# Performance work log

Measured on AMD Instinct MI355X. Metric: run time of the kernel, lower is better.

Reference implementation:

```python
import math
import jax, jax.numpy as jnp
import numpy as np

B, S, HID = 1, 2048, 2880
H, HKV, D = 64, 8, 64
G = H // HKV  # num_key_value_groups = 8


def setup_inputs() -> dict:
    key = jax.random.key(0)
    ks = jax.random.split(key, 10)
    sd = 1.0 / math.sqrt(HID)
    hidden_states = jax.random.normal(ks[0], (B, S, HID), dtype=jnp.float32)
    # causal additive mask [B, 1, S, S]
    causal = jnp.tril(jnp.ones((S, S), dtype=bool))
    attention_mask = jnp.where(causal, 0.0, -1e9).astype(jnp.float32)[None, None]
    Wq = jax.random.normal(ks[1], (H * D, HID), dtype=jnp.float32) * sd
    bq = jax.random.normal(ks[2], (H * D,), dtype=jnp.float32) * 0.01
    Wk = jax.random.normal(ks[3], (HKV * D, HID), dtype=jnp.float32) * sd
    bk = jax.random.normal(ks[4], (HKV * D,), dtype=jnp.float32) * 0.01
    Wv = jax.random.normal(ks[5], (HKV * D, HID), dtype=jnp.float32) * sd
    bv = jax.random.normal(ks[6], (HKV * D,), dtype=jnp.float32) * 0.01
    Wo = jax.random.normal(ks[7], (HID, H * D), dtype=jnp.float32) * (1.0 / math.sqrt(H * D))
    bo = jax.random.normal(ks[8], (HID,), dtype=jnp.float32) * 0.01
    return {"hidden_states": hidden_states, "attention_mask": attention_mask,
            "Wq": Wq, "bq": bq, "Wk": Wk, "bk": bk, "Wv": Wv, "bv": bv,
            "Wo": Wo, "bo": bo}


def reference(hidden_states, attention_mask, Wq, bq, Wk, bk, Wv, bv, Wo, bo):
    b, s, _ = hidden_states.shape
    # projections
    q = hidden_states @ Wq.T + bq  # [b, s, H*D]
    k = hidden_states @ Wk.T + bk  # [b, s, HKV*D]
    v = hidden_states @ Wv.T + bv
    # torch q head index h maps to kv head h // G, so split H -> (HKV, G)
    q = q.reshape(b, s, HKV, G, D).transpose(0, 2, 3, 1, 4)   # [b, kv, g, s, d]
    k = k.reshape(b, s, HKV, D).transpose(0, 2, 1, 3)         # [b, kv, s, d]
    v = v.reshape(b, s, HKV, D).transpose(0, 2, 1, 3)
    # grouped-query attention without materializing repeated KV (same math as repeat_interleave)
    scores = jnp.einsum('bkgsd,bktd->bkgst', q, k) / math.sqrt(D)
    scores = scores + attention_mask[:, :, None]              # broadcast [b,1,1,s,t]
    attn = jax.nn.softmax(scores.astype(jnp.float32), axis=-1).astype(q.dtype)
    out = jnp.einsum('bkgst,bktd->bkgsd', attn, v)            # [b, kv, g, s, d]
    out = out.transpose(0, 3, 1, 2, 4).reshape(b, s, H * D)
    return out @ Wo.T + bo
```

## Files before the change

kernel.cpp:

```cpp
#include <hip/hip_runtime.h>
#include <hip/hip_bf16.h>
#include <cmath>

typedef __hip_bfloat16 bf16;
typedef __bf16 bf16x8 __attribute__((ext_vector_type(8)));
typedef float floatx4 __attribute__((ext_vector_type(4)));

__device__ inline floatx4 mfma16(bf16x8 a, bf16x8 b, floatx4 c) {
  return __builtin_amdgcn_mfma_f32_16x16x32_bf16(a, b, c, 0, 0, 0);
}

__device__ inline void async_ld16(const void* g, void* l) {
  __builtin_amdgcn_global_load_lds((const __attribute__((address_space(1))) void*)g,
                                   (__attribute__((address_space(3))) void*)l,
                                   16, 0, 0);
}

__device__ inline uint4 pack8(float4 a, float4 b) {
  union { uint4 u; bf16 h[8]; } t;
  t.h[0] = __float2bfloat16(a.x); t.h[1] = __float2bfloat16(a.y);
  t.h[2] = __float2bfloat16(a.z); t.h[3] = __float2bfloat16(a.w);
  t.h[4] = __float2bfloat16(b.x); t.h[5] = __float2bfloat16(b.y);
  t.h[6] = __float2bfloat16(b.z); t.h[7] = __float2bfloat16(b.w);
  return t.u;
}

__global__ __launch_bounds__(256)
void cvt_f32_bf16(const float* __restrict__ s, bf16* __restrict__ d, int n8) {
  const int i = blockIdx.x * 256 + threadIdx.x;
  if (i >= n8) return;
  const float4 a = ((const float4*)s)[2 * i];
  const float4 b = ((const float4*)s)[2 * i + 1];
  ((uint4*)d)[i] = pack8(a, b);
}

__global__ void concat_bias3(const float* __restrict__ q, const float* __restrict__ k,
                             const float* __restrict__ v, float* __restrict__ o) {
  const int i = blockIdx.x * 256 + threadIdx.x;
  if (i < 4096) o[i] = q[i];
  else if (i < 4608) o[i] = k[i - 4096];
  else o[i] = v[i - 4608];
}

#define QSCALE 0.1803368801111601f

template <int A_BF, int B_BF, int OUT_MODE>
__global__ __launch_bounds__(256)
void gemm_bt_bias(const void* __restrict__ Ap, const void* __restrict__ Bp,
                  const float* __restrict__ bias, void* __restrict__ Cp,
                  void* __restrict__ Cqp, void* __restrict__ Ctp,
                  int M, int N, int K, float qmul) {
  __shared__ __align__(16) bf16 sA[128 * 32];
  __shared__ __align__(16) bf16 sB[128 * 32];
  const int tid  = threadIdx.x;
  const int wave = tid >> 6;
  const int lane = tid & 63;
  const int quad = lane >> 4;
  const int l15  = lane & 15;
  const int bm = blockIdx.y * 128;
  const int bn = blockIdx.x * 128;
  const int wm = (wave & 1) * 64;
  const int wn = (wave >> 1) * 64;

  floatx4 acc[4][4] = {};

  const int g0 = tid, g1 = tid + 256;
  const int arow0 = bm + (g0 >> 2), acol0 = (g0 & 3) * 8;
  const int arow1 = bm + (g1 >> 2), acol1 = (g1 & 3) * 8;
  int brow0 = bn + (g0 >> 2); if (brow0 >= N) brow0 = N - 1;
  int brow1 = bn + (g1 >> 2); if (brow1 >= N) brow1 = N - 1;

  for (int k0 = 0; k0 < K; k0 += 32) {
    __syncthreads();
    if (A_BF) {
      const bf16* A = (const bf16*)Ap;
      async_ld16(A + (size_t)arow0 * K + k0 + acol0, sA + wave * 512);
      async_ld16(A + (size_t)arow1 * K + k0 + acol1, sA + 2048 + wave * 512);
    } else {
      const float* A = (const float*)Ap;
      const float* p0 = A + (size_t)arow0 * K + k0 + acol0;
      const float* p1 = A + (size_t)arow1 * K + k0 + acol1;
      *(uint4*)(sA + tid * 8)        = pack8(*(const float4*)p0, *(const float4*)(p0 + 4));
      *(uint4*)(sA + 2048 + tid * 8) = pack8(*(const float4*)p1, *(const float4*)(p1 + 4));
    }
    if (B_BF) {
      const bf16* B = (const bf16*)Bp;
      async_ld16(B + (size_t)brow0 * K + k0 + acol0, sB + wave * 512);
      async_ld16(B + (size_t)brow1 * K + k0 + acol1, sB + 2048 + wave * 512);
    } else {
      const float* B = (const float*)Bp;
      const float* p0 = B + (size_t)brow0 * K + k0 + acol0;
      const float* p1 = B + (size_t)brow1 * K + k0 + acol1;
      *(uint4*)(sB + tid * 8)        = pack8(*(const float4*)p0, *(const float4*)(p0 + 4));
      *(uint4*)(sB + 2048 + tid * 8) = pack8(*(const float4*)p1, *(const float4*)(p1 + 4));
    }
    __syncthreads();

    bf16x8 aF[4], bF[4];
#pragma unroll
    for (int mi = 0; mi < 4; ++mi)
      aF[mi] = *(const bf16x8*)(sA + (wm + mi * 16 + l15) * 32 + quad * 8);
#pragma unroll
    for (int ni = 0; ni < 4; ++ni)
      bF[ni] = *(const bf16x8*)(sB + (wn + ni * 16 + l15) * 32 + quad * 8);
#pragma unroll
    for (int mi = 0; mi < 4; ++mi)
#pragma unroll
      for (int ni = 0; ni < 4; ++ni)
        acc[mi][ni] = mfma16(aF[mi], bF[ni], acc[mi][ni]);
  }

#pragma unroll
  for (int ni = 0; ni < 4; ++ni) {
    const int col = bn + wn + ni * 16 + l15;
    if (col >= N) continue;
    const float bv = bias[col];
#pragma unroll
    for (int mi = 0; mi < 4; ++mi) {
      const int row = bm + wm + mi * 16 + quad * 4;
#pragma unroll
      for (int r = 0; r < 4; ++r) {
        const float val = acc[mi][ni][r] + bv;
        if (OUT_MODE == 0) {
          ((bf16*)Cp)[(size_t)(row + r) * N + col] = __float2bfloat16(val * qmul);
        } else if (OUT_MODE == 1) {
          ((float*)Cp)[(size_t)(row + r) * N + col] = val;
        } else if (OUT_MODE == 2) {
          ((bf16*)Ctp)[(size_t)col * M + row + r] = __float2bfloat16(val);
        } else {
          if (col < 4096)      ((bf16*)Cp)[(size_t)(row + r) * 4096 + col] = __float2bfloat16(val * qmul);
          else if (col < 4608) ((bf16*)Cqp)[(size_t)(row + r) * 512 + (col - 4096)] = __float2bfloat16(val);
          else                 ((bf16*)Ctp)[(size_t)(col - 4608) * M + row + r] = __float2bfloat16(val);
        }
      }
    }
  }
}

__global__ __launch_bounds__(256)
void attn_fused(const bf16* __restrict__ Q, const bf16* __restrict__ Kc,
                const bf16* __restrict__ Vt, bf16* __restrict__ AO) {
  constexpr int HD = 4096, KD = 512, SEQ = 2048;
  constexpr float NEG = -1e30f;
  __shared__ __align__(16) bf16 sP[64 * 64];
  __shared__ __align__(16) bf16 sK[2][64 * 64];
  __shared__ __align__(16) bf16 sV[2][64 * 64];

  const int qb = (int)gridDim.x - 1 - blockIdx.x;
  const int h  = blockIdx.y;
  const int kvh = h >> 3;
  const int tid = threadIdx.x, wave = tid >> 6, lane = tid & 63;
  const int quad = lane >> 4, l15 = lane & 15;
  const int sq0 = qb * 64;

  const int lrow = lane >> 3;
  const int lgr  = (lane & 7) ^ lrow;

  bf16x8 qf[2];
#pragma unroll
  for (int ks = 0; ks < 2; ++ks)
    qf[ks] = *(const bf16x8*)(Q + (size_t)(sq0 + wave * 16 + l15) * HD + h * 64 + ks * 32 + quad * 8);

  bf16x8 onesf;
#pragma unroll
  for (int i = 0; i < 8; ++i) onesf[i] = (__bf16)1.0f;

#pragma unroll
  for (int i = 0; i < 2; ++i) {
    const int c = wave * 2 + i;
    async_ld16(Kc + (size_t)(c * 8 + lrow) * KD + kvh * 64 + lgr * 8, &sK[0][c * 512]);
    async_ld16(Vt + (size_t)(kvh * 64 + c * 8 + lrow) * SEQ + lgr * 8, &sV[0][c * 512]);
  }

  floatx4 o_acc[4] = {};
  floatx4 o_sum = {};
  float m_run = NEG;

  for (int kt = 0; kt <= qb; ++kt) {
    const int st0 = kt * 64;
    __syncthreads();

    if (kt < qb) {
      const int st1 = st0 + 64;
      const int nb = (kt + 1) & 1;
#pragma unroll
      for (int i = 0; i < 2; ++i) {
        const int c = wave * 2 + i;
        async_ld16(Kc + (size_t)(st1 + c * 8 + lrow) * KD + kvh * 64 + lgr * 8, &sK[nb][c * 512]);
        async_ld16(Vt + (size_t)(kvh * 64 + c * 8 + lrow) * SEQ + st1 + lgr * 8, &sV[nb][c * 512]);
      }
    }
    const bf16* kb = sK[kt & 1];
    const bf16* vb = sV[kt & 1];

    floatx4 s_acc[4] = {};
#pragma unroll
    for (int ks = 0; ks < 2; ++ks) {
#pragma unroll
      for (int ni = 0; ni < 4; ++ni) {
        const bf16x8 kF = *(const bf16x8*)(kb + (ni * 16 + l15) * 64 + (((ks * 4 + quad) ^ (l15 & 7)) * 8));
        s_acc[ni] = mfma16(kF, qf[ks], s_acc[ni]);
      }
    }

    if (kt == qb) {
      const int qloc = wave * 16 + l15;
#pragma unroll
      for (int ni = 0; ni < 4; ++ni)
#pragma unroll
        for (int r = 0; r < 4; ++r)
          if (ni * 16 + quad * 4 + r > qloc) s_acc[ni][r] = NEG;
    }

    float t0 = fmaxf(fmaxf(s_acc[0][0], s_acc[0][1]), fmaxf(s_acc[0][2], s_acc[0][3]));
    float t1 = fmaxf(fmaxf(s_acc[1][0], s_acc[1][1]), fmaxf(s_acc[1][2], s_acc[1][3]));
    float t2 = fmaxf(fmaxf(s_acc[2][0], s_acc[2][1]), fmaxf(s_acc[2][2], s_acc[2][3]));
    float t3 = fmaxf(fmaxf(s_acc[3][0], s_acc[3][1]), fmaxf(s_acc[3][2], s_acc[3][3]));
    float tm = fmaxf(fmaxf(t0, t1), fmaxf(t2, t3));
    tm = fmaxf(tm, __shfl_xor(tm, 16));
    tm = fmaxf(tm, __shfl_xor(tm, 32));

    if (!__all(tm - m_run <= 8.0f)) {
      const float mn = fmaxf(m_run, tm);
      const float alpha = exp2f(m_run - mn);
      m_run = mn;
#pragma unroll
      for (int r = 0; r < 4; ++r) o_sum[r] *= alpha;
#pragma unroll
      for (int di = 0; di < 4; ++di)
#pragma unroll
        for (int r = 0; r < 4; ++r) o_acc[di][r] *= alpha;
    }

    const int prow = wave * 16 + l15;
#pragma unroll
    for (int ni = 0; ni < 4; ++ni) {
      union { uint2 u; bf16 hh[4]; } pk;
#pragma unroll
      for (int r = 0; r < 4; ++r)
        pk.hh[r] = __float2bfloat16(exp2f(s_acc[ni][r] - m_run));
      const int g = ni * 2 + (quad >> 1);
      *(uint2*)(sP + prow * 64 + ((g ^ (l15 & 7)) * 8) + (quad & 1) * 4) = pk.u;
    }

#pragma unroll
    for (int ks = 0; ks < 2; ++ks) {
      const bf16x8 pF = *(const bf16x8*)(sP + prow * 64 + (((ks * 4 + quad) ^ (l15 & 7)) * 8));
#pragma unroll
      for (int di = 0; di < 4; ++di) {
        const bf16x8 vF = *(const bf16x8*)(vb + (di * 16 + l15) * 64 + (((ks * 4 + quad) ^ (l15 & 7)) * 8));
        o_acc[di] = mfma16(vF, pF, o_acc[di]);
      }
      o_sum = mfma16(onesf, pF, o_sum);
    }
  }

  const float inv = 1.0f / o_sum[0];
  const int row = sq0 + wave * 16 + l15;
#pragma unroll
  for (int di = 0; di < 4; ++di) {
    union { uint2 u; bf16 hh[4]; } pk;
#pragma unroll
    for (int r = 0; r < 4; ++r)
      pk.hh[r] = __float2bfloat16(o_acc[di][r] * inv);
    *(uint2*)(AO + (size_t)row * HD + h * 64 + di * 16 + quad * 4) = pk.u;
  }
}

extern "C" void kernel_launch(void* const* d_in, const int* in_sizes, int n_in,
                              void* d_out, int out_size, void* d_ws, size_t ws_size,
                              hipStream_t stream) {
  const float* X  = (const float*)d_in[0];
  const float* Wq = (const float*)d_in[2];
  const float* bq = (const float*)d_in[3];
  const float* Wk = (const float*)d_in[4];
  const float* bk = (const float*)d_in[5];
  const float* Wv = (const float*)d_in[6];
  const float* bv = (const float*)d_in[7];
  const float* Wo = (const float*)d_in[8];
  const float* bo = (const float*)d_in[9];
  float* out = (float*)d_out;

  char* ws = (char*)d_ws;
  bf16* Qb = (bf16*)(ws);
  bf16* Kb = (bf16*)(ws + 16777216);
  bf16* Vt = (bf16*)(ws + 18874368);
  bf16* AO = (bf16*)(ws + 20971520);
  bf16*  Xb   = (bf16*)(ws + 37748736);
  bf16*  Wall = (bf16*)(ws + 49545216);
  bf16*  Wob  = (bf16*)(ws + 79036416);
  float* ball = (float*)(ws + 102629376);
  const size_t NEED = 102649856;

  dim3 blk(256);
  if (ws_size >= NEED) {
    cvt_f32_bf16<<<dim3(2048 * 2880 / 8 / 256), blk, 0, stream>>>(X, Xb, 2048 * 2880 / 8);
    cvt_f32_bf16<<<dim3(4096 * 2880 / 8 / 256), blk, 0, stream>>>(Wq, Wall, 4096 * 2880 / 8);
    cvt_f32_bf16<<<dim3(512 * 2880 / 8 / 256),  blk, 0, stream>>>(Wk, Wall + (size_t)4096 * 2880, 512 * 2880 / 8);
    cvt_f32_bf16<<<dim3(512 * 2880 / 8 / 256),  blk, 0, stream>>>(Wv, Wall + (size_t)4608 * 2880, 512 * 2880 / 8);
    cvt_f32_bf16<<<dim3(2880 * 4096 / 8 / 256), blk, 0, stream>>>(Wo, Wob, 2880 * 4096 / 8);
    concat_bias3<<<dim3(20), blk, 0, stream>>>(bq, bk, bv, ball);

    gemm_bt_bias<1, 1, 4><<<dim3(40, 16), blk, 0, stream>>>(Xb, Wall, ball, Qb, Kb, Vt, 2048, 5120, 2880, QSCALE);
    attn_fused<<<dim3(32, 64), blk, 0, stream>>>(Qb, Kb, Vt, AO);
    gemm_bt_bias<1, 1, 1><<<dim3(23, 16), blk, 0, stream>>>(AO, Wob, bo, out, nullptr, nullptr, 2048, 2880, 4096, 1.f);
  } else {
    gemm_bt_bias<0, 0, 0><<<dim3(32, 16), blk, 0, stream>>>(X, Wq, bq, Qb, nullptr, nullptr, 2048, 4096, 2880, QSCALE);
    gemm_bt_bias<0, 0, 0><<<dim3(4, 16),  blk, 0, stream>>>(X, Wk, bk, Kb, nullptr, nullptr, 2048, 512, 2880, 1.f);
    gemm_bt_bias<0, 0, 2><<<dim3(4, 16),  blk, 0, stream>>>(X, Wv, bv, nullptr, nullptr, Vt, 2048, 512, 2880, 1.f);
    attn_fused<<<dim3(32, 64), blk, 0, stream>>>(Qb, Kb, Vt, AO);
    gemm_bt_bias<1, 0, 1><<<dim3(23, 16), blk, 0, stream>>>(AO, Wo, bo, out, nullptr, nullptr, 2048, 2880, 4096, 1.f);
  }
}
```

Baseline: 513.0 us.

## Add double-buffered bf16 GEMM with XCD-aware block remap and remap attention grid

Adds a new bf16 GEMM kernel that double-buffers the A/B LDS tiles, issuing async global-to-LDS loads for the next K step while MFMAs run on the current one, with a single barrier per iteration. It also remaps workgroup indices so that consecutive tiles land on the same XCD (lin&7 striding), and applies the same remap to the attention grid. Both fast-path GEMMs now use it. The aim is to hide load latency and improve L2 locality, at the cost of doubled LDS use (lower occupancy) and a reliance on the ordering of the async loads against the barrier.

```diff
diff --git a/kernel.cpp b/kernel.cpp
--- a/kernel.cpp
+++ b/kernel.cpp
@@ -43,6 +43,93 @@
 }
 
 #define QSCALE 0.1803368801111601f
+
+template <int OUT_MODE>
+__global__ __launch_bounds__(256)
+void gemm_bt_db(const bf16* __restrict__ A, const bf16* __restrict__ B,
+                const float* __restrict__ bias, void* __restrict__ Cp,
+                void* __restrict__ Cqp, void* __restrict__ Ctp,
+                int M, int N, int K, float qmul) {
+  __shared__ __align__(16) bf16 sA[2][128 * 32];
+  __shared__ __align__(16) bf16 sB[2][128 * 32];
+  const int tid  = threadIdx.x;
+  const int wave = tid >> 6;
+  const int lane = tid & 63;
+  const int quad = lane >> 4;
+  const int l15  = lane & 15;
+
+  const int nwg = gridDim.x * gridDim.y;
+  const int lin = blockIdx.y * gridDim.x + blockIdx.x;
+  const int L   = (lin & 7) * (nwg >> 3) + (lin >> 3);
+  const int bm  = (L / gridDim.x) * 128;
+  const int bn  = (L % gridDim.x) * 128;
+
+  const int wm = (wave & 1) * 64;
+  const int wn = (wave >> 1) * 64;
+
+  floatx4 acc[4][4] = {};
+
+  const int g0 = tid, g1 = tid + 256;
+  const int arow0 = bm + (g0 >> 2), acol0 = (g0 & 3) * 8;
+  const int arow1 = bm + (g1 >> 2), acol1 = (g1 & 3) * 8;
+  int brow0 = bn + (g0 >> 2); if (brow0 >= N) brow0 = N - 1;
+  int brow1 = bn + (g1 >> 2); if (brow1 >= N) brow1 = N - 1;
+
+  const int nk = K >> 5;
+  async_ld16(A + (size_t)arow0 * K + acol0, &sA[0][wave * 512]);
+  async_ld16(A + (size_t)arow1 * K + acol1, &sA[0][2048 + wave * 512]);
+  async_ld16(B + (size_t)brow0 * K + acol0, &sB[0][wave * 512]);
+  async_ld16(B + (size_t)brow1 * K + acol1, &sB[0][2048 + wave * 512]);
+
+  for (int kt = 0; kt < nk; ++kt) {
+    __syncthreads();
+    if (kt + 1 < nk) {
+      const int k0 = (kt + 1) << 5;
+      const int nb = (kt + 1) & 1;
+      async_ld16(A + (size_t)arow0 * K + k0 + acol0, &sA[nb][wave * 512]);
+      async_ld16(A + (size_t)arow1 * K + k0 + acol1, &sA[nb][2048 + wave * 512]);
+      async_ld16(B + (size_t)brow0 * K + k0 + acol0, &sB[nb][wave * 512]);
+      async_ld16(B + (size_t)brow1 * K + k0 + acol1, &sB[nb][2048 + wave * 512]);
+    }
+    const bf16* a = sA[kt & 1];
+    const bf16* b = sB[kt & 1];
+
+    bf16x8 aF[4], bF[4];
+#pragma unroll
+    for (int mi = 0; mi < 4; ++mi)
+      aF[mi] = *(const bf16x8*)(a + (wm + mi * 16 + l15) * 32 + quad * 8);
+#pragma unroll
+    for (int ni = 0; ni < 4; ++ni)
+      bF[ni] = *(const bf16x8*)(b + (wn + ni * 16 + l15) * 32 + quad * 8);
+#pragma unroll
+    for (int mi = 0; mi < 4; ++mi)
+#pragma unroll
+      for (int ni = 0; ni < 4; ++ni)
+        acc[mi][ni] = mfma16(aF[mi], bF[ni], acc[mi][ni]);
+  }
+
+#pragma unroll
+  for (int ni = 0; ni < 4; ++ni) {
+    const int col = bn + wn + ni * 16 + l15;
+    if (col >= N) continue;
+    const float bv = bias[col];
+#pragma unroll
+    for (int mi = 0; mi < 4; ++mi) {
+      const int row = bm + wm + mi * 16 + quad * 4;
+#pragma unroll
+      for (int r = 0; r < 4; ++r) {
+        const float val = acc[mi][ni][r] + bv;
+        if (OUT_MODE == 1) {
+          ((float*)Cp)[(size_t)(row + r) * N + col] = val;
+        } else {
+          if (col < 4096)      ((bf16*)Cp)[(size_t)(row + r) * 4096 + col] = __float2bfloat16(val * qmul);
+          else if (col < 4608) ((bf16*)Cqp)[(size_t)(row + r) * 512 + (col - 4096)] = __float2bfloat16(val);
+          else                 ((bf16*)Ctp)[(size_t)(col - 4608) * M + row + r] = __float2bfloat16(val);
+        }
+      }
+    }
+  }
+}
 
 template <int A_BF, int B_BF, int OUT_MODE>
 __global__ __launch_bounds__(256)
@@ -127,10 +214,6 @@
           ((float*)Cp)[(size_t)(row + r) * N + col] = val;
         } else if (OUT_MODE == 2) {
           ((bf16*)Ctp)[(size_t)col * M + row + r] = __float2bfloat16(val);
-        } else {
-          if (col < 4096)      ((bf16*)Cp)[(size_t)(row + r) * 4096 + col] = __float2bfloat16(val * qmul);
-          else if (col < 4608) ((bf16*)Cqp)[(size_t)(row + r) * 512 + (col - 4096)] = __float2bfloat16(val);
-          else                 ((bf16*)Ctp)[(size_t)(col - 4608) * M + row + r] = __float2bfloat16(val);
         }
       }
     }
@@ -146,8 +229,10 @@
   __shared__ __align__(16) bf16 sK[2][64 * 64];
   __shared__ __align__(16) bf16 sV[2][64 * 64];
 
-  const int qb = (int)gridDim.x - 1 - blockIdx.x;
-  const int h  = blockIdx.y;
+  const int lin = blockIdx.y * 32 + blockIdx.x;
+  const int L   = (lin & 7) * 256 + (lin >> 3);
+  const int h   = L >> 5;
+  const int qb  = 31 - (L & 31);
   const int kvh = h >> 3;
   const int tid = threadIdx.x, wave = tid >> 6, lane = tid & 63;
   const int quad = lane >> 4, l15 = lane & 15;
@@ -301,9 +386,9 @@
     cvt_f32_bf16<<<dim3(2880 * 4096 / 8 / 256), blk, 0, stream>>>(Wo, Wob, 2880 * 4096 / 8);
     concat_bias3<<<dim3(20), blk, 0, stream>>>(bq, bk, bv, ball);
 
-    gemm_bt_bias<1, 1, 4><<<dim3(40, 16), blk, 0, stream>>>(Xb, Wall, ball, Qb, Kb, Vt, 2048, 5120, 2880, QSCALE);
+    gemm_bt_db<4><<<dim3(40, 16), blk, 0, stream>>>(Xb, Wall, ball, Qb, Kb, Vt, 2048, 5120, 2880, QSCALE);
     attn_fused<<<dim3(32, 64), blk, 0, stream>>>(Qb, Kb, Vt, AO);
-    gemm_bt_bias<1, 1, 1><<<dim3(23, 16), blk, 0, stream>>>(AO, Wob, bo, out, nullptr, nullptr, 2048, 2880, 4096, 1.f);
+    gemm_bt_db<1><<<dim3(23, 16), blk, 0, stream>>>(AO, Wob, bo, out, nullptr, nullptr, 2048, 2880, 4096, 1.f);
   } else {
     gemm_bt_bias<0, 0, 0><<<dim3(32, 16), blk, 0, stream>>>(X, Wq, bq, Qb, nullptr, nullptr, 2048, 4096, 2880, QSCALE);
     gemm_bt_bias<0, 0, 0><<<dim3(4, 16),  blk, 0, stream>>>(X, Wk, bk, Kb, nullptr, nullptr, 2048, 512, 2880, 1.f);
```

Result: faster. 447.9 us (-12.7%).
